# Optimization experiments

Measured on AMD Instinct MI355X. Metric: run time of the kernel, lower is better.

Reference implementation:

```python
import jax, jax.numpy as jnp
import numpy as np

N = 100000      # nodes
E = 1600000     # edges (without self loops)
G = 64          # graphs in batch
H = 4           # attention heads
C = 42          # hidden dim per head (node_hidden_dim)
DIN = 42        # node_input_dim
NEG_SLOPE = 0.2  # PyG GATConv default


def setup_inputs() -> dict:
    key = jax.random.key(0)
    ks = jax.random.split(key, 24)
    x = jax.random.normal(ks[0], (N, DIN), jnp.float32)
    # edges with src != dst (GATConv removes then re-adds self loops; we emulate
    # by generating loop-free edges and appending self loops in reference())
    src = jax.random.randint(ks[1], (E,), 0, N, dtype=jnp.int32)
    off = jax.random.randint(ks[2], (E,), 1, N, dtype=jnp.int32)
    dst = ((src + off) % N).astype(jnp.int32)
    edge_index = jnp.stack([src, dst])
    batch = jnp.sort(jax.random.randint(ks[3], (N,), 0, G, dtype=jnp.int32))
    s = 0.1
    inp = {
        'x': x, 'edge_index': edge_index, 'batch': batch,
        'lin0_w': s * jax.random.normal(ks[4], (DIN, C), jnp.float32),
        'lin0_b': jnp.zeros((C,), jnp.float32),
    }
    ins = [C, H * C, H * C]  # layer input widths: 42, 168, 168
    for l in range(3):
        inp[f'W{l+1}'] = s * jax.random.normal(ks[5 + 4 * l], (ins[l], H * C), jnp.float32)
        inp[f'asrc{l+1}'] = s * jax.random.normal(ks[6 + 4 * l], (H, C), jnp.float32)
        inp[f'adst{l+1}'] = s * jax.random.normal(ks[7 + 4 * l], (H, C), jnp.float32)
        inp[f'b{l+1}'] = jnp.zeros((H * C,), jnp.float32)
    return inp


def _gat_layer(x, src, dst, W, a_src, a_dst, bias):
    # x: [N, Fin] -> h: [N, H, C]
    h = (x @ W).reshape(N, H, C)
    alpha_src = jnp.sum(h * a_src[None], axis=-1)  # [N, H]
    alpha_dst = jnp.sum(h * a_dst[None], axis=-1)  # [N, H]
    e = jax.nn.leaky_relu(alpha_src[src] + alpha_dst[dst], NEG_SLOPE)  # [E', H]
    # segment softmax over incoming edges of each destination node
    m = jax.ops.segment_max(e, dst, num_segments=N)
    m = jnp.where(jnp.isfinite(m), m, 0.0)
    ex = jnp.exp(e - m[dst])
    denom = jax.ops.segment_sum(ex, dst, num_segments=N)
    alpha = ex / denom[dst]  # self loops guarantee denom > 0
    out = jax.ops.segment_sum(h[src] * alpha[:, :, None], dst, num_segments=N)
    return out.reshape(N, H * C) + bias


def reference(x, edge_index, batch, lin0_w, lin0_b,
              W1, asrc1, adst1, b1,
              W2, asrc2, adst2, b2,
              W3, asrc3, adst3, b3):
    x = jax.nn.elu(x @ lin0_w + lin0_b)
    loops = jnp.arange(N, dtype=edge_index.dtype)
    src = jnp.concatenate([edge_index[0], loops])
    dst = jnp.concatenate([edge_index[1], loops])
    for W, a_s, a_d, b in ((W1, asrc1, adst1, b1),
                           (W2, asrc2, adst2, b2),
                           (W3, asrc3, adst3, b3)):
        x = jax.nn.elu(_gat_layer(x, src, dst, W, a_s, a_d, b))
        # dropout p=0.0 -> identity; residual in original is computed but unused
    counts = jax.ops.segment_sum(jnp.ones((N,), x.dtype), batch, num_segments=G)
    sums = jax.ops.segment_sum(x, batch, num_segments=G)
    return sums / jnp.maximum(counts, 1.0)[:, None]  # [G, H*C]
```

## Files before the change

### kernel.cpp

```cpp
#include <hip/hip_runtime.h>
#include <hip/hip_fp16.h>
#include <cstdint>

#define HC 168
#define CC 42
#define NH 4
#define NP 84
#define AP 192
#define A0P 64
#define NEG 0.2f

typedef _Float16 f16;
typedef __attribute__((ext_vector_type(8))) _Float16 f16x8;
typedef __attribute__((ext_vector_type(4))) float f32x4;

__device__ __forceinline__ float lrelu(float v) { return fmaxf(v, NEG * v); }
__device__ __forceinline__ float eluf(float v)  { return v > 0.f ? v : __expf(v) - 1.f; }

__device__ __forceinline__ float sel4(float4 w, int h) {
  float r = w.x;
  r = (h == 1) ? w.y : r;
  r = (h == 2) ? w.z : r;
  r = (h == 3) ? w.w : r;
  return r;
}

__global__ __launch_bounds__(256) void gemm0_kernel(
    const float* __restrict__ X, const float* __restrict__ W,
    const float* __restrict__ bias, f16* __restrict__ Out,
    int N, int Fin, int Ncols, int pitch) {
  __shared__ float xs[128][CC];
  __shared__ float ws[CC][64];
  const int row0 = blockIdx.x * 128;
  const int col0 = blockIdx.y * 64;
  const int tid = threadIdx.x;
  const int tr = tid >> 4;
  const int tc = tid & 15;
  float acc[8][4];
#pragma unroll
  for (int r = 0; r < 8; ++r)
#pragma unroll
    for (int c = 0; c < 4; ++c) acc[r][c] = 0.f;

  for (int k0 = 0; k0 < Fin; k0 += CC) {
    for (int i = tid; i < 128 * CC; i += 256) {
      int r = i / CC, k = i - r * CC;
      int gr = row0 + r;
      xs[r][k] = (gr < N) ? X[(int64_t)gr * Fin + k0 + k] : 0.f;
    }
    for (int i = tid; i < CC * 64; i += 256) {
      int k = i >> 6, c = i & 63;
      int gc = col0 + c;
      ws[k][c] = (gc < Ncols) ? W[(k0 + k) * Ncols + gc] : 0.f;
    }
    __syncthreads();
#pragma unroll 6
    for (int k = 0; k < CC; ++k) {
      float4 w4 = *(const float4*)&ws[k][tc * 4];
#pragma unroll
      for (int r = 0; r < 8; ++r) {
        float xv = xs[tr * 8 + r][k];
        acc[r][0] += xv * w4.x; acc[r][1] += xv * w4.y;
        acc[r][2] += xv * w4.z; acc[r][3] += xv * w4.w;
      }
    }
    __syncthreads();
  }
#pragma unroll
  for (int r = 0; r < 8; ++r) {
    int gr = row0 + tr * 8 + r;
    if (gr >= N) continue;
#pragma unroll
    for (int c = 0; c < 4; ++c) {
      int gc = col0 + tc * 4 + c;
      if (gc < pitch) {
        f16 o = (f16)0.f;
        if (gc < Ncols) o = (f16)eluf(acc[r][c] + bias[gc]);
        Out[(int64_t)gr * pitch + gc] = o;
      }
    }
  }
}

__global__ void wconv_kernel(const float* __restrict__ W, f16* __restrict__ Wf,
                             int Fin, int KCN) {
  int i = blockIdx.x * 256 + threadIdx.x;
  int tot = 11 * KCN * 64;
  if (i >= tot) return;
  int lane = i & 63;
  int t = i >> 6;
  int kc = t % KCN;
  int ct = t / KCN;
  int r = lane & 15, g = lane >> 4;
  int col = ct * 16 + r;
  f16 vals[8];
#pragma unroll
  for (int j = 0; j < 8; ++j) {
    int k = kc * 32 + g * 8 + j;
    float v = (k < Fin && col < HC) ? W[k * HC + col] : 0.f;
    vals[j] = (f16)v;
  }
  *(f16x8*)(Wf + (size_t)i * 8) = *(f16x8*)vals;
}

template<int KCN>
__global__ __launch_bounds__(256) void mfma_gemm_kernel(
    const f16* __restrict__ A, const f16* __restrict__ Wf,
    f16* __restrict__ Out, int N) {
  const int lane = threadIdx.x & 63;
  const int wid = (blockIdx.x * 256 + threadIdx.x) >> 6;
  const int row0 = wid * 16;
  if (row0 >= N) return;
  const int r = lane & 15, g = lane >> 4;
  f16x8 a[KCN];
  const f16* ap = A + (int64_t)(row0 + r) * (KCN * 32) + g * 8;
#pragma unroll
  for (int kc = 0; kc < KCN; ++kc)
    a[kc] = *(const f16x8*)(ap + kc * 32);
  f16* op = Out + (int64_t)row0 * HC;
#pragma unroll
  for (int ct = 0; ct < 11; ++ct) {
    f32x4 acc = {0.f, 0.f, 0.f, 0.f};
#pragma unroll
    for (int kc = 0; kc < KCN; ++kc) {
      f16x8 b = *(const f16x8*)(Wf + (((size_t)ct * KCN + kc) * 64 + lane) * 8);
      acc = __builtin_amdgcn_mfma_f32_16x16x32_f16(a[kc], b, acc, 0, 0, 0);
    }
    const int col = ct * 16 + r;
    if (col < HC) {
#pragma unroll
      for (int v = 0; v < 4; ++v)
        op[(int64_t)(g * 4 + v) * HC + col] = (f16)acc[v];
    }
  }
}

__global__ void alpha_kernel(const __half2* __restrict__ H2,
                             const float* __restrict__ asrc,
                             const float* __restrict__ adst,
                             float* __restrict__ as_, float* __restrict__ ad_,
                             int N) {
  int i = blockIdx.x * 256 + threadIdx.x;
  if (i >= N * NH) return;
  int n = i >> 2, h = i & 3;
  const __half2* hp = H2 + (int64_t)n * NP + h * (CC / 2);
  const float* ap = asrc + h * CC;
  const float* bp = adst + h * CC;
  float s = 0.f, d = 0.f;
#pragma unroll 7
  for (int j = 0; j < CC / 2; ++j) {
    float2 f = __half22float2(hp[j]);
    s += f.x * ap[2 * j] + f.y * ap[2 * j + 1];
    d += f.x * bp[2 * j] + f.y * bp[2 * j + 1];
  }
  as_[i] = s; ad_[i] = d;
}

__global__ void zero_i_kernel(int* __restrict__ p, int n) {
  int i = blockIdx.x * 256 + threadIdx.x;
  if (i < n) p[i] = 0;
}

__global__ void hist_kernel(const int* __restrict__ dst, int* __restrict__ cnt, int E) {
  int e = blockIdx.x * 256 + threadIdx.x;
  if (e < E) atomicAdd(&cnt[dst[e]], 1);
}

__global__ __launch_bounds__(256) void scan1_kernel(
    const int* __restrict__ cnt, int* __restrict__ rp1, int* __restrict__ blksum, int N) {
  __shared__ int lds[256];
  int t = threadIdx.x;
  int base = blockIdx.x * 1024 + t * 4;
  int v0 = (base + 0 < N) ? cnt[base + 0] : 0;
  int v1 = (base + 1 < N) ? cnt[base + 1] : 0;
  int v2 = (base + 2 < N) ? cnt[base + 2] : 0;
  int v3 = (base + 3 < N) ? cnt[base + 3] : 0;
  v1 += v0; v2 += v1; v3 += v2;
  lds[t] = v3;
  __syncthreads();
  for (int off = 1; off < 256; off <<= 1) {
    int add = (t >= off) ? lds[t - off] : 0;
    __syncthreads();
    lds[t] += add;
    __syncthreads();
  }
  int excl = lds[t] - v3;
  if (base + 0 < N) rp1[base + 0] = excl + v0;
  if (base + 1 < N) rp1[base + 1] = excl + v1;
  if (base + 2 < N) rp1[base + 2] = excl + v2;
  if (base + 3 < N) rp1[base + 3] = excl + v3;
  if (t == 255) blksum[blockIdx.x] = lds[255];
}

__global__ __launch_bounds__(256) void scan2_kernel(int* __restrict__ blksum, int nblk) {
  __shared__ int lds[256];
  int t = threadIdx.x;
  int v = (t < nblk) ? blksum[t] : 0;
  lds[t] = v;
  __syncthreads();
  for (int off = 1; off < 256; off <<= 1) {
    int add = (t >= off) ? lds[t - off] : 0;
    __syncthreads();
    lds[t] += add;
    __syncthreads();
  }
  if (t < nblk) blksum[t] = lds[t] - v;
}

__global__ void scan3_kernel(const int* __restrict__ blksum, int* __restrict__ rp1,
                             int* __restrict__ row_ptr0, int* __restrict__ cnt_cursor, int N) {
  int i = blockIdx.x * 256 + threadIdx.x;
  if (i >= N) return;
  int incl = rp1[i] + blksum[i >> 10];
  rp1[i] = incl;
  cnt_cursor[i] = incl - cnt_cursor[i];
  if (i == 0) row_ptr0[0] = 0;
}

__global__ void scatter_kernel(const int* __restrict__ src, const int* __restrict__ dst,
                               int* __restrict__ cursor, int* __restrict__ src_sorted, int E) {
  int e = blockIdx.x * 256 + threadIdx.x;
  if (e >= E) return;
  int pos = atomicAdd(&cursor[dst[e]], 1);
  src_sorted[pos] = src[e];
}

__global__ __launch_bounds__(256) void gat_agg_kernel(
    const int* __restrict__ row_ptr, const int* __restrict__ src_sorted,
    const __half2* __restrict__ H2, const float4* __restrict__ as4,
    const float4* __restrict__ ad4_, const float* __restrict__ bias,
    __half* __restrict__ out, int N) {
  __shared__ int    lidx[4][64];
  __shared__ float4 lw[4][64];
  const int wv = threadIdx.x >> 6;
  const int lane = threadIdx.x & 63;
  const int wid = (blockIdx.x * 256 + threadIdx.x) >> 6;
  if (wid >= N) return;
  const int n = wid;
  const bool act = (lane < 42);
  const int p0 = 2 * lane;
  const int hX = p0 / 21;
  const int hY = (p0 + 1) / 21;
  const float4 adn = ad4_[n];
  float ax0 = 0.f, ay0 = 0.f, ax1 = 0.f, ay1 = 0.f, denA = 0.f, denB = 0.f;

#define GAT_ACC(s_, wX_, wY_)                                               \
  {                                                                         \
    denA += wX_; denB += wY_;                                               \
    if (act) {                                                              \
      float2 raw = *(const float2*)(H2 + (int64_t)(s_) * NP + p0);          \
      __half2 u0 = *(__half2*)&raw.x, u1 = *(__half2*)&raw.y;               \
      float2 f0 = __half22float2(u0), f1 = __half22float2(u1);              \
      ax0 += f0.x * wX_; ay0 += f0.y * wX_;                                 \
      ax1 += f1.x * wY_; ay1 += f1.y * wY_;                                 \
    }                                                                       \
  }

  {
    const float4 a4 = as4[n];
    float4 w4 = make_float4(__expf(lrelu(a4.x + adn.x)), __expf(lrelu(a4.y + adn.y)),
                            __expf(lrelu(a4.z + adn.z)), __expf(lrelu(a4.w + adn.w)));
    float wX = sel4(w4, hX), wY = sel4(w4, hY);
    GAT_ACC(n, wX, wY);
  }

  const int beg = row_ptr[n], end = row_ptr[n + 1];
  for (int base = beg; base < end; base += 64) {
    const int m = min(64, end - base);
    int idx = (lane < m) ? src_sorted[base + lane] : n;
    float4 a4 = as4[idx];
    float4 w4 = make_float4(__expf(lrelu(a4.x + adn.x)), __expf(lrelu(a4.y + adn.y)),
                            __expf(lrelu(a4.z + adn.z)), __expf(lrelu(a4.w + adn.w)));
    lidx[wv][lane] = idx;
    lw[wv][lane] = w4;

#define GAT_EDGE(jj)                                                        \
    {                                                                       \
      int s = lidx[wv][jj];                                                 \
      float4 ww = lw[wv][jj];                                               \
      float wX = sel4(ww, hX), wY = sel4(ww, hY);                           \
      GAT_ACC(s, wX, wY);                                                   \
    }

    int j = 0;
    for (; j + 4 <= m; j += 4) {
      GAT_EDGE(j) GAT_EDGE(j + 1) GAT_EDGE(j + 2) GAT_EDGE(j + 3)
    }
    for (; j < m; ++j) GAT_EDGE(j)
#undef GAT_EDGE
  }
#undef GAT_ACC

  if (act) {
    float4 b4 = *(const float4*)(bias + 4 * lane);
    union { __half h[4]; uint2 u; } ob;
    ob.h[0] = __float2half(eluf(ax0 / denA + b4.x));
    ob.h[1] = __float2half(eluf(ay0 / denA + b4.y));
    ob.h[2] = __float2half(eluf(ax1 / denB + b4.z));
    ob.h[3] = __float2half(eluf(ay1 / denB + b4.w));
    *(uint2*)(out + (int64_t)n * AP + 4 * lane) = ob.u;
  } else if (lane < 48) {
    *(uint2*)(out + (int64_t)n * AP + 4 * lane) = make_uint2(0u, 0u);
  }
}

__global__ void gbound_kernel(const int* __restrict__ batch, int* __restrict__ gstart,
                              int N, int G) {
  int i = blockIdx.x * 256 + threadIdx.x;
  if (i > N) return;
  if (i == 0) {
    for (int g = 0; g <= batch[0]; ++g) gstart[g] = 0;
  } else if (i == N) {
    for (int g = batch[N - 1] + 1; g <= G; ++g) gstart[g] = N;
  } else {
    int a = batch[i - 1], b = batch[i];
    for (int g = a + 1; g <= b; ++g) gstart[g] = i;
  }
}

__global__ void zero_f_kernel(float* __restrict__ p, int n) {
  int i = blockIdx.x * 256 + threadIdx.x;
  if (i < n) p[i] = 0.f;
}

#define PSPLIT 4
__global__ __launch_bounds__(192) void pool2_kernel(
    const __half* __restrict__ x, const int* __restrict__ gstart,
    float* __restrict__ sums, int G) {
  int g = blockIdx.x;
  int t = threadIdx.x;
  if (t >= HC) return;
  int beg = gstart[g], end = gstart[g + 1];
  float s = 0.f;
  for (int n = beg + (int)blockIdx.y; n < end; n += PSPLIT)
    s += __half2float(x[(int64_t)n * AP + t]);
  atomicAdd(sums + g * HC + t, s);
}

__global__ void out2_kernel(const float* __restrict__ sums, const int* __restrict__ gstart,
                            float* __restrict__ out, int G) {
  int i = blockIdx.x * 256 + threadIdx.x;
  if (i >= G * HC) return;
  int g = i / HC;
  float cnt = (float)(gstart[g + 1] - gstart[g]);
  out[i] = sums[i] / fmaxf(cnt, 1.f);
}

static inline int cdiv(int64_t a, int b) { return (int)((a + b - 1) / b); }

extern "C" void kernel_launch(void* const* d_in, const int* in_sizes, int n_in,
                              void* d_out, int out_size, void* d_ws, size_t ws_size,
                              hipStream_t stream) {
  const float* x      = (const float*)d_in[0];
  const int*   eidx   = (const int*)d_in[1];
  const int*   batch  = (const int*)d_in[2];
  const float* lin0_w = (const float*)d_in[3];
  const float* lin0_b = (const float*)d_in[4];
  const float* W[3]  = {(const float*)d_in[5],  (const float*)d_in[9],  (const float*)d_in[13]};
  const float* As[3] = {(const float*)d_in[6],  (const float*)d_in[10], (const float*)d_in[14]};
  const float* Ad[3] = {(const float*)d_in[7],  (const float*)d_in[11], (const float*)d_in[15]};
  const float* Bi[3] = {(const float*)d_in[8],  (const float*)d_in[12], (const float*)d_in[16]};

  const int N = in_sizes[2];
  const int E = in_sizes[1] / 2;
  const int G = out_size / HC;
  const int* src = eidx;
  const int* dst = eidx + E;

  char* p = (char*)d_ws;
  f16* act0 = (f16*)p;  p += (size_t)N * A0P * 2;
  f16* actv = (f16*)p;  p += (size_t)N * AP * 2;
  f16* h16  = (f16*)p;  p += (size_t)N * HC * 2;
  f16* Wf1  = (f16*)p;  p += (size_t)11 * 2 * 64 * 8 * 2;
  f16* Wf2  = (f16*)p;  p += (size_t)11 * 6 * 64 * 8 * 2;
  f16* Wf3  = (f16*)p;  p += (size_t)11 * 6 * 64 * 8 * 2;
  float* as_  = (float*)p; p += (size_t)N * NH * 4;
  float* ad_  = (float*)p; p += (size_t)N * NH * 4;
  float* sums = (float*)p; p += (size_t)G * HC * 4;
  int* gstart     = (int*)p; p += (size_t)(G + 1) * 4;
  int* row_ptr    = (int*)p; p += (size_t)(N + 1) * 4;
  int* cursor     = (int*)p; p += (size_t)N * 4;
  int* blksum     = (int*)p; p += 256 * 4;
  int* src_sorted = (int*)p; p += (size_t)E * 4;
  (void)ws_size;

  const __half2* H2 = (const __half2*)h16;
  const int nblk = cdiv(N, 1024);
  const int mfma_blocks = cdiv(cdiv(N, 16), 4);

  gemm0_kernel<<<dim3(cdiv(N, 128), cdiv(A0P, 64)), 256, 0, stream>>>(
      x, lin0_w, lin0_b, act0, N, CC, CC, A0P);

  wconv_kernel<<<cdiv(11 * 2 * 64, 256), 256, 0, stream>>>(W[0], Wf1, CC, 2);
  wconv_kernel<<<cdiv(11 * 6 * 64, 256), 256, 0, stream>>>(W[1], Wf2, HC, 6);
  wconv_kernel<<<cdiv(11 * 6 * 64, 256), 256, 0, stream>>>(W[2], Wf3, HC, 6);

  zero_i_kernel<<<cdiv(N, 256), 256, 0, stream>>>(cursor, N);
  hist_kernel<<<cdiv(E, 256), 256, 0, stream>>>(dst, cursor, E);
  scan1_kernel<<<nblk, 256, 0, stream>>>(cursor, row_ptr + 1, blksum, N);
  scan2_kernel<<<1, 256, 0, stream>>>(blksum, nblk);
  scan3_kernel<<<cdiv(N, 256), 256, 0, stream>>>(blksum, row_ptr + 1, row_ptr, cursor, N);
  scatter_kernel<<<cdiv(E, 256), 256, 0, stream>>>(src, dst, cursor, src_sorted, E);

  gbound_kernel<<<cdiv(N + 1, 256), 256, 0, stream>>>(batch, gstart, N, G);

  for (int l = 0; l < 3; ++l) {
    if (l == 0) {
      mfma_gemm_kernel<2><<<mfma_blocks, 256, 0, stream>>>(act0, Wf1, h16, N);
    } else {
      mfma_gemm_kernel<6><<<mfma_blocks, 256, 0, stream>>>(actv, (l == 1) ? Wf2 : Wf3, h16, N);
    }
    alpha_kernel<<<cdiv((int64_t)N * NH, 256), 256, 0, stream>>>(
        (const __half2*)h16, As[l], Ad[l], as_, ad_, N);
    gat_agg_kernel<<<cdiv(N, 4), 256, 0, stream>>>(
        row_ptr, src_sorted, H2, (const float4*)as_, (const float4*)ad_, Bi[l],
        (__half*)actv, N);
  }

  zero_f_kernel<<<cdiv(G * HC, 256), 256, 0, stream>>>(sums, G * HC);
  pool2_kernel<<<dim3(G, PSPLIT), 192, 0, stream>>>((const __half*)actv, gstart, sums, G);
  out2_kernel<<<cdiv(G * HC, 256), 256, 0, stream>>>(sums, gstart, (float*)d_out, G);
}
```

Before: 886.0 us.

## Pad per-head features to 44 and move input linear layer onto MFMA

Per-head hidden features are padded from 42 to 44 columns (row pitch 176), so each lane in the aggregation kernel covers four features of a single head. That removes the per-edge two-head weight selection and halves the denominator tracking. The edge loop is unrolled by 8 and stores precomputed byte offsets and per-head weights in shared memory. The fp32 SIMT lin0 GEMM is replaced by an fp16 cast kernel plus an MFMA GEMM, and the weight-conversion kernel gains padding-aware remapping for inputs and outputs. The trade-off is more bytes per gathered row, an extra cast pass, and fp16 rounding of the input layer.

```diff
diff --git a/kernel.cpp b/kernel.cpp
--- a/kernel.cpp
+++ b/kernel.cpp
@@ -5,7 +5,9 @@
 #define HC 168
 #define CC 42
 #define NH 4
-#define NP 84
+#define PH 44
+#define HP 176
+#define HPB 352
 #define AP 192
 #define A0P 64
 #define NEG 0.2f
@@ -25,86 +27,72 @@
   return r;
 }
 
-__global__ __launch_bounds__(256) void gemm0_kernel(
-    const float* __restrict__ X, const float* __restrict__ W,
-    const float* __restrict__ bias, f16* __restrict__ Out,
-    int N, int Fin, int Ncols, int pitch) {
-  __shared__ float xs[128][CC];
-  __shared__ float ws[CC][64];
-  const int row0 = blockIdx.x * 128;
-  const int col0 = blockIdx.y * 64;
-  const int tid = threadIdx.x;
-  const int tr = tid >> 4;
-  const int tc = tid & 15;
-  float acc[8][4];
-#pragma unroll
-  for (int r = 0; r < 8; ++r)
-#pragma unroll
-    for (int c = 0; c < 4; ++c) acc[r][c] = 0.f;
-
-  for (int k0 = 0; k0 < Fin; k0 += CC) {
-    for (int i = tid; i < 128 * CC; i += 256) {
-      int r = i / CC, k = i - r * CC;
-      int gr = row0 + r;
-      xs[r][k] = (gr < N) ? X[(int64_t)gr * Fin + k0 + k] : 0.f;
-    }
-    for (int i = tid; i < CC * 64; i += 256) {
-      int k = i >> 6, c = i & 63;
-      int gc = col0 + c;
-      ws[k][c] = (gc < Ncols) ? W[(k0 + k) * Ncols + gc] : 0.f;
-    }
-    __syncthreads();
-#pragma unroll 6
-    for (int k = 0; k < CC; ++k) {
-      float4 w4 = *(const float4*)&ws[k][tc * 4];
-#pragma unroll
-      for (int r = 0; r < 8; ++r) {
-        float xv = xs[tr * 8 + r][k];
-        acc[r][0] += xv * w4.x; acc[r][1] += xv * w4.y;
-        acc[r][2] += xv * w4.z; acc[r][3] += xv * w4.w;
-      }
-    }
-    __syncthreads();
-  }
-#pragma unroll
-  for (int r = 0; r < 8; ++r) {
-    int gr = row0 + tr * 8 + r;
-    if (gr >= N) continue;
-#pragma unroll
-    for (int c = 0; c < 4; ++c) {
-      int gc = col0 + tc * 4 + c;
-      if (gc < pitch) {
-        f16 o = (f16)0.f;
-        if (gc < Ncols) o = (f16)eluf(acc[r][c] + bias[gc]);
-        Out[(int64_t)gr * pitch + gc] = o;
-      }
-    }
-  }
+__global__ void cast16_kernel(const float* __restrict__ X, f16* __restrict__ O, int N) {
+  int i = blockIdx.x * 256 + threadIdx.x;
+  if (i >= N * A0P) return;
+  int n = i >> 6, c = i & 63;
+  O[i] = (c < CC) ? (f16)X[n * CC + c] : (f16)0.f;
 }
 
 __global__ void wconv_kernel(const float* __restrict__ W, f16* __restrict__ Wf,
-                             int Fin, int KCN) {
-  int i = blockIdx.x * 256 + threadIdx.x;
-  int tot = 11 * KCN * 64;
+                             int NCT, int KCN, int kpad, int Fink, int cpad, int Ncols,
+                             int wstride) {
+  int i = blockIdx.x * 256 + threadIdx.x;
+  int tot = NCT * KCN * 64;
   if (i >= tot) return;
   int lane = i & 63;
   int t = i >> 6;
   int kc = t % KCN;
   int ct = t / KCN;
-  int r = lane & 15, g = lane >> 4;
-  int col = ct * 16 + r;
+  int cl = ct * 16 + (lane & 15);
+  int corig; bool cok;
+  if (cpad) { int h = cl / PH, c = cl % PH; cok = (c < CC && h < NH); corig = h * CC + c; }
+  else      { cok = (cl < Ncols); corig = cl; }
   f16 vals[8];
 #pragma unroll
   for (int j = 0; j < 8; ++j) {
-    int k = kc * 32 + g * 8 + j;
-    float v = (k < Fin && col < HC) ? W[k * HC + col] : 0.f;
-    vals[j] = (f16)v;
+    int kp = kc * 32 + (lane >> 4) * 8 + j;
+    int korig; bool kok;
+    if (kpad) { int h = kp / PH, c = kp % PH; kok = (c < CC && h < NH && kp < HP); korig = h * CC + c; }
+    else      { kok = (kp < Fink); korig = kp; }
+    vals[j] = (kok && cok) ? (f16)W[korig * wstride + corig] : (f16)0.f;
   }
   *(f16x8*)(Wf + (size_t)i * 8) = *(f16x8*)vals;
 }
 
+__global__ __launch_bounds__(256) void mfma_gemm0_kernel(
+    const f16* __restrict__ A, const f16* __restrict__ Wf,
+    const float* __restrict__ bias, f16* __restrict__ Out, int N) {
+  const int lane = threadIdx.x & 63;
+  const int wid = (blockIdx.x * 256 + threadIdx.x) >> 6;
+  const int row0 = wid * 16;
+  if (row0 >= N) return;
+  const int r = lane & 15, g = lane >> 4;
+  f16x8 a[2];
+  const f16* ap = A + (int64_t)(row0 + r) * A0P + g * 8;
+#pragma unroll
+  for (int kc = 0; kc < 2; ++kc) a[kc] = *(const f16x8*)(ap + kc * 32);
+  f16* op = Out + (int64_t)row0 * A0P;
+#pragma unroll
+  for (int ct = 0; ct < 4; ++ct) {
+    f32x4 acc = {0.f, 0.f, 0.f, 0.f};
+#pragma unroll
+    for (int kc = 0; kc < 2; ++kc) {
+      f16x8 b = *(const f16x8*)(Wf + (((size_t)ct * 2 + kc) * 64 + lane) * 8);
+      acc = __builtin_amdgcn_mfma_f32_16x16x32_f16(a[kc], b, acc, 0, 0, 0);
+    }
+    const int col = ct * 16 + r;
+    float bv = (col < CC) ? bias[col] : 0.f;
+#pragma unroll
+    for (int v = 0; v < 4; ++v) {
+      f16 o = (col < CC) ? (f16)eluf(acc[v] + bv) : (f16)0.f;
+      op[(int64_t)(g * 4 + v) * A0P + col] = o;
+    }
+  }
+}
+
 template<int KCN>
-__global__ __launch_bounds__(256) void mfma_gemm_kernel(
+__global__ __launch_bounds__(256) void mfma_gemmL_kernel(
     const f16* __restrict__ A, const f16* __restrict__ Wf,
     f16* __restrict__ Out, int N) {
   const int lane = threadIdx.x & 63;
@@ -115,9 +103,8 @@
   f16x8 a[KCN];
   const f16* ap = A + (int64_t)(row0 + r) * (KCN * 32) + g * 8;
 #pragma unroll
-  for (int kc = 0; kc < KCN; ++kc)
-    a[kc] = *(const f16x8*)(ap + kc * 32);
-  f16* op = Out + (int64_t)row0 * HC;
+  for (int kc = 0; kc < KCN; ++kc) a[kc] = *(const f16x8*)(ap + kc * 32);
+  f16* op = Out + (int64_t)row0 * HP;
 #pragma unroll
   for (int ct = 0; ct < 11; ++ct) {
     f32x4 acc = {0.f, 0.f, 0.f, 0.f};
@@ -127,11 +114,9 @@
       acc = __builtin_amdgcn_mfma_f32_16x16x32_f16(a[kc], b, acc, 0, 0, 0);
     }
     const int col = ct * 16 + r;
-    if (col < HC) {
-#pragma unroll
-      for (int v = 0; v < 4; ++v)
-        op[(int64_t)(g * 4 + v) * HC + col] = (f16)acc[v];
-    }
+#pragma unroll
+    for (int v = 0; v < 4; ++v)
+      op[(int64_t)(g * 4 + v) * HP + col] = (f16)acc[v];
   }
 }
 
@@ -143,7 +128,7 @@
   int i = blockIdx.x * 256 + threadIdx.x;
   if (i >= N * NH) return;
   int n = i >> 2, h = i & 3;
-  const __half2* hp = H2 + (int64_t)n * NP + h * (CC / 2);
+  const __half2* hp = H2 + (int64_t)n * (HP / 2) + h * (PH / 2);
   const float* ap = asrc + h * CC;
   const float* bp = adst + h * CC;
   float s = 0.f, d = 0.f;
@@ -227,32 +212,31 @@
 
 __global__ __launch_bounds__(256) void gat_agg_kernel(
     const int* __restrict__ row_ptr, const int* __restrict__ src_sorted,
-    const __half2* __restrict__ H2, const float4* __restrict__ as4,
+    const f16* __restrict__ H16, const float4* __restrict__ as4,
     const float4* __restrict__ ad4_, const float* __restrict__ bias,
-    __half* __restrict__ out, int N) {
-  __shared__ int    lidx[4][64];
-  __shared__ float4 lw[4][64];
+    f16* __restrict__ out, int N) {
+  __shared__ int   loff[4][64];
+  __shared__ float lw4[4][64][4];
   const int wv = threadIdx.x >> 6;
   const int lane = threadIdx.x & 63;
   const int wid = (blockIdx.x * 256 + threadIdx.x) >> 6;
   if (wid >= N) return;
   const int n = wid;
-  const bool act = (lane < 42);
-  const int p0 = 2 * lane;
-  const int hX = p0 / 21;
-  const int hY = (p0 + 1) / 21;
+  const bool act = (lane < 44);
+  const int hL = act ? (lane / 11) : 0;
+  const int myoff = lane * 8;
   const float4 adn = ad4_[n];
-  float ax0 = 0.f, ay0 = 0.f, ax1 = 0.f, ay1 = 0.f, denA = 0.f, denB = 0.f;
-
-#define GAT_ACC(s_, wX_, wY_)                                               \
+  float ax = 0.f, ay = 0.f, az = 0.f, aw = 0.f, den = 0.f;
+
+#define GAT_ACC(boff_, w_)                                                  \
   {                                                                         \
-    denA += wX_; denB += wY_;                                               \
+    den += w_;                                                              \
     if (act) {                                                              \
-      float2 raw = *(const float2*)(H2 + (int64_t)(s_) * NP + p0);          \
+      float2 raw = *(const float2*)((const char*)H16 + (boff_) + myoff);    \
       __half2 u0 = *(__half2*)&raw.x, u1 = *(__half2*)&raw.y;               \
       float2 f0 = __half22float2(u0), f1 = __half22float2(u1);              \
-      ax0 += f0.x * wX_; ay0 += f0.y * wX_;                                 \
-      ax1 += f1.x * wY_; ay1 += f1.y * wY_;                                 \
+      ax += f0.x * w_; ay += f0.y * w_;                                     \
+      az += f1.x * w_; aw += f1.y * w_;                                     \
     }                                                                       \
   }
 
@@ -260,8 +244,8 @@
     const float4 a4 = as4[n];
     float4 w4 = make_float4(__expf(lrelu(a4.x + adn.x)), __expf(lrelu(a4.y + adn.y)),
                             __expf(lrelu(a4.z + adn.z)), __expf(lrelu(a4.w + adn.w)));
-    float wX = sel4(w4, hX), wY = sel4(w4, hY);
-    GAT_ACC(n, wX, wY);
+    float w = sel4(w4, hL);
+    GAT_ACC((int64_t)n * HPB, w);
   }
 
   const int beg = row_ptr[n], end = row_ptr[n + 1];
@@ -271,36 +255,39 @@
     float4 a4 = as4[idx];
     float4 w4 = make_float4(__expf(lrelu(a4.x + adn.x)), __expf(lrelu(a4.y + adn.y)),
                             __expf(lrelu(a4.z + adn.z)), __expf(lrelu(a4.w + adn.w)));
-    lidx[wv][lane] = idx;
-    lw[wv][lane] = w4;
+    loff[wv][lane] = idx * HPB;
+    *(float4*)&lw4[wv][lane][0] = w4;
 
 #define GAT_EDGE(jj)                                                        \
     {                                                                       \
-      int s = lidx[wv][jj];                                                 \
-      float4 ww = lw[wv][jj];                                               \
-      float wX = sel4(ww, hX), wY = sel4(ww, hY);                           \
-      GAT_ACC(s, wX, wY);                                                   \
+      int boff = loff[wv][jj];                                              \
+      float w = lw4[wv][jj][hL];                                            \
+      GAT_ACC((int64_t)boff, w);                                            \
     }
 
     int j = 0;
-    for (; j + 4 <= m; j += 4) {
-      GAT_EDGE(j) GAT_EDGE(j + 1) GAT_EDGE(j + 2) GAT_EDGE(j + 3)
+    for (; j + 8 <= m; j += 8) {
+      GAT_EDGE(j)     GAT_EDGE(j + 1) GAT_EDGE(j + 2) GAT_EDGE(j + 3)
+      GAT_EDGE(j + 4) GAT_EDGE(j + 5) GAT_EDGE(j + 6) GAT_EDGE(j + 7)
     }
     for (; j < m; ++j) GAT_EDGE(j)
 #undef GAT_EDGE
   }
 #undef GAT_ACC
 
-  if (act) {
-    float4 b4 = *(const float4*)(bias + 4 * lane);
-    union { __half h[4]; uint2 u; } ob;
-    ob.h[0] = __float2half(eluf(ax0 / denA + b4.x));
-    ob.h[1] = __float2half(eluf(ay0 / denA + b4.y));
-    ob.h[2] = __float2half(eluf(ax1 / denB + b4.z));
-    ob.h[3] = __float2half(eluf(ay1 / denB + b4.w));
-    *(uint2*)(out + (int64_t)n * AP + 4 * lane) = ob.u;
-  } else if (lane < 48) {
-    *(uint2*)(out + (int64_t)n * AP + 4 * lane) = make_uint2(0u, 0u);
+  if (lane < 48) {
+    f16 o[4] = {(f16)0.f, (f16)0.f, (f16)0.f, (f16)0.f};
+    if (act) {
+      const int q = lane - hL * 11;
+      const float acc[4] = {ax, ay, az, aw};
+      const float rden = 1.f / den;
+#pragma unroll
+      for (int t = 0; t < 4; ++t) {
+        int c = q * 4 + t;
+        if (c < CC) o[t] = (f16)eluf(acc[t] * rden + bias[hL * CC + c]);
+      }
+    }
+    *(uint2*)(out + (int64_t)n * AP + lane * 4) = *(uint2*)o;
   }
 }
 
@@ -325,15 +312,16 @@
 
 #define PSPLIT 4
 __global__ __launch_bounds__(192) void pool2_kernel(
-    const __half* __restrict__ x, const int* __restrict__ gstart,
+    const f16* __restrict__ x, const int* __restrict__ gstart,
     float* __restrict__ sums, int G) {
   int g = blockIdx.x;
   int t = threadIdx.x;
   if (t >= HC) return;
+  int pos = (t / CC) * PH + t % CC;
   int beg = gstart[g], end = gstart[g + 1];
   float s = 0.f;
   for (int n = beg + (int)blockIdx.y; n < end; n += PSPLIT)
-    s += __half2float(x[(int64_t)n * AP + t]);
+    s += (float)x[(int64_t)n * AP + pos];
   atomicAdd(sums + g * HC + t, s);
 }
 
@@ -368,9 +356,11 @@
   const int* dst = eidx + E;
 
   char* p = (char*)d_ws;
+  f16* x16  = (f16*)p;  p += (size_t)N * A0P * 2;
   f16* act0 = (f16*)p;  p += (size_t)N * A0P * 2;
   f16* actv = (f16*)p;  p += (size_t)N * AP * 2;
-  f16* h16  = (f16*)p;  p += (size_t)N * HC * 2;
+  f16* h16  = (f16*)p;  p += (size_t)N * HP * 2;
+  f16* Wf0  = (f16*)p;  p += (size_t)4 * 2 * 64 * 8 * 2;
   f16* Wf1  = (f16*)p;  p += (size_t)11 * 2 * 64 * 8 * 2;
   f16* Wf2  = (f16*)p;  p += (size_t)11 * 6 * 64 * 8 * 2;
   f16* Wf3  = (f16*)p;  p += (size_t)11 * 6 * 64 * 8 * 2;
@@ -384,16 +374,16 @@
   int* src_sorted = (int*)p; p += (size_t)E * 4;
   (void)ws_size;
 
-  const __half2* H2 = (const __half2*)h16;
   const int nblk = cdiv(N, 1024);
   const int mfma_blocks = cdiv(cdiv(N, 16), 4);
 
-  gemm0_kernel<<<dim3(cdiv(N, 128), cdiv(A0P, 64)), 256, 0, stream>>>(
-      x, lin0_w, lin0_b, act0, N, CC, CC, A0P);
-
-  wconv_kernel<<<cdiv(11 * 2 * 64, 256), 256, 0, stream>>>(W[0], Wf1, CC, 2);
-  wconv_kernel<<<cdiv(11 * 6 * 64, 256), 256, 0, stream>>>(W[1], Wf2, HC, 6);
-  wconv_kernel<<<cdiv(11 * 6 * 64, 256), 256, 0, stream>>>(W[2], Wf3, HC, 6);
+  cast16_kernel<<<cdiv((int64_t)N * A0P, 256), 256, 0, stream>>>(x, x16, N);
+  wconv_kernel<<<cdiv(4 * 2 * 64, 256),  256, 0, stream>>>(lin0_w, Wf0, 4, 2, 0, CC, 0, CC, CC);
+  wconv_kernel<<<cdiv(11 * 2 * 64, 256), 256, 0, stream>>>(W[0], Wf1, 11, 2, 0, CC, 1, HC, HC);
+  wconv_kernel<<<cdiv(11 * 6 * 64, 256), 256, 0, stream>>>(W[1], Wf2, 11, 6, 1, HC, 1, HC, HC);
+  wconv_kernel<<<cdiv(11 * 6 * 64, 256), 256, 0, stream>>>(W[2], Wf3, 11, 6, 1, HC, 1, HC, HC);
+
+  mfma_gemm0_kernel<<<mfma_blocks, 256, 0, stream>>>(x16, Wf0, lin0_b, act0, N);
 
   zero_i_kernel<<<cdiv(N, 256), 256, 0, stream>>>(cursor, N);
   hist_kernel<<<cdiv(E, 256), 256, 0, stream>>>(dst, cursor, E);
@@ -405,19 +395,17 @@
   gbound_kernel<<<cdiv(N + 1, 256), 256, 0, stream>>>(batch, gstart, N, G);
 
   for (int l = 0; l < 3; ++l) {
-    if (l == 0) {
-      mfma_gemm_kernel<2><<<mfma_blocks, 256, 0, stream>>>(act0, Wf1, h16, N);
-    } else {
-      mfma_gemm_kernel<6><<<mfma_blocks, 256, 0, stream>>>(actv, (l == 1) ? Wf2 : Wf3, h16, N);
-    }
+    if (l == 0)
+      mfma_gemmL_kernel<2><<<mfma_blocks, 256, 0, stream>>>(act0, Wf1, h16, N);
+    else
+      mfma_gemmL_kernel<6><<<mfma_blocks, 256, 0, stream>>>(actv, (l == 1) ? Wf2 : Wf3, h16, N);
     alpha_kernel<<<cdiv((int64_t)N * NH, 256), 256, 0, stream>>>(
         (const __half2*)h16, As[l], Ad[l], as_, ad_, N);
     gat_agg_kernel<<<cdiv(N, 4), 256, 0, stream>>>(
-        row_ptr, src_sorted, H2, (const float4*)as_, (const float4*)ad_, Bi[l],
-        (__half*)actv, N);
+        row_ptr, src_sorted, h16, (const float4*)as_, (const float4*)ad_, Bi[l], actv, N);
   }
 
   zero_f_kernel<<<cdiv(G * HC, 256), 256, 0, stream>>>(sums, G * HC);
-  pool2_kernel<<<dim3(G, PSPLIT), 192, 0, stream>>>((const __half*)actv, gstart, sums, G);
+  pool2_kernel<<<dim3(G, PSPLIT), 192, 0, stream>>>(actv, gstart, sums, G);
   out2_kernel<<<cdiv(G * HC, 256), 256, 0, stream>>>(sums, gstart, (float*)d_out, G);
 }
```

New measurement: 887.6 us. Within noise of the previous version (+0.2%).
